# Kernel optimization log

Measured on AMD Instinct MI355X. Metric: run time of the kernel, lower is better.

## Reference

```python
import jax, jax.numpy as jnp
import numpy as np

B, H, W, C = 3072, 64, 64, 3  # kernel_size=64 forces H=W=64; reshape forces B % 3 == 0


def setup_inputs() -> dict:
    key = jax.random.key(0)
    k0, k1, k2, k3, k4 = jax.random.split(key, 5)
    inputs = jax.random.normal(k0, (B, H, W, C), dtype=jnp.float32)
    # Conv2D(filters=3, kernel_size=64) params, HWIO layout
    w1 = jax.random.normal(k1, (64, 64, 3, 3), dtype=jnp.float32) * 0.02
    b1 = jax.random.normal(k2, (3,), dtype=jnp.float32) * 0.02
    w2 = jax.random.normal(k3, (64, 64, 3, 3), dtype=jnp.float32) * 0.02
    b2 = jax.random.normal(k4, (3,), dtype=jnp.float32) * 0.02
    return {"inputs": inputs, "w1": w1, "b1": b1, "w2": w2, "b2": b2}


def _hilbert_axis1(x):
    # FFT-based Hilbert transform along axis=1 (analytic-signal filter), N even
    N = x.shape[1]
    h = np.zeros(N, dtype=np.float32)
    h[0] = h[N // 2] = 1.0
    h[1:N // 2] = 2.0
    hf = jnp.asarray(h)[None, :, None, None]
    Xf = jnp.fft.fft(x, axis=1)
    return jnp.imag(jnp.fft.ifft(Xf * hf, axis=1)).astype(x.dtype)


def reference(inputs, w1, b1, w2, b2):
    maps_x = inputs[..., :3]                                  # [B,64,64,3]
    b_, h_, w_, c_ = maps_x.shape
    # kernel covers the whole 64x64 image -> 1x1 conv output == full contraction
    v1 = jnp.einsum('bhwc,hwcf->bf', maps_x, w1) + b1          # [B,3]
    v2 = jnp.einsum('bhwc,hwcf->bf', maps_x, w2) + b2          # [B,3]
    V = jnp.stack([v1, v2], axis=-1)                           # [B,3,2]
    V = V / (1e-6 + jnp.sum(jnp.abs(V), axis=1, keepdims=True))
    mx_t = maps_x.reshape(b_, h_ * w_, c_).transpose(0, 2, 1)  # [B,3,HW]
    # Gram matrix and closed-form 2x2 inverse (math of tf.linalg.inv on [B,2,2])
    G = jnp.einsum('bci,bcj->bij', V, V)                       # [B,2,2]
    a = G[:, 0, 0]; bb = G[:, 0, 1]; c = G[:, 1, 0]; d = G[:, 1, 1]
    det = a * d - bb * c
    Ginv = jnp.stack([jnp.stack([d, -bb], -1),
                      jnp.stack([-c, a], -1)], 1) / det[:, None, None]  # [B,2,2]
    Vt_x = jnp.einsum('bck,bcn->bkn', V, mx_t)                 # [B,2,HW]
    rec_t = jnp.einsum('bck,bkn->bcn', V, Ginv @ Vt_x)         # [B,3,HW]
    # lstsq(V, rec_t) via normal equations (tf fast lstsq): z = Ginv V^T rec_t
    z = Ginv @ jnp.einsum('bck,bcn->bkn', V, rec_t)            # [B,2,HW]
    rec = z.transpose(0, 2, 1).reshape(-1, h_, w_, c_)         # [2B/3,64,64,3]
    rec_h = _hilbert_axis1(rec)
    return jnp.concatenate([rec, rec_h], axis=-1)              # [2B/3,64,64,6]
```

## Files before the change

### kernel.cpp

```cpp
#include <hip/hip_runtime.h>
#include <math.h>

#define B_TOT 3072
#define PIX   12288
#define BM    4

typedef float v2f __attribute__((ext_vector_type(2)));

__global__ __launch_bounds__(256) void compute_M_kernel(
    const float* __restrict__ x, const float* __restrict__ w1,
    const float* __restrict__ b1, const float* __restrict__ w2,
    const float* __restrict__ b2, float* __restrict__ Mout) {
  const int b0 = blockIdx.x * BM;
  const float4* __restrict__ w14 = (const float4*)w1;
  const float4* __restrict__ w24 = (const float4*)w2;
  const float4* __restrict__ xb4 = (const float4*)(x + (size_t)b0 * PIX);

  float acc[BM][6];
  #pragma unroll
  for (int b = 0; b < BM; ++b)
    #pragma unroll
    for (int f = 0; f < 6; ++f) acc[b][f] = 0.f;

  #pragma unroll 2
  for (int it = 0; it < PIX / 4 / 256; ++it) {
    const int i4 = threadIdx.x + it * 256;
    float4 a0 = w14[i4 * 3 + 0], a1 = w14[i4 * 3 + 1], a2 = w14[i4 * 3 + 2];
    float4 c0 = w24[i4 * 3 + 0], c1 = w24[i4 * 3 + 1], c2 = w24[i4 * 3 + 2];
    #pragma unroll
    for (int b = 0; b < BM; ++b) {
      float4 xv = xb4[(size_t)b * (PIX / 4) + i4];
      acc[b][0] += xv.x * a0.x + xv.y * a0.w + xv.z * a1.z + xv.w * a2.y;
      acc[b][1] += xv.x * a0.y + xv.y * a1.x + xv.z * a1.w + xv.w * a2.z;
      acc[b][2] += xv.x * a0.z + xv.y * a1.y + xv.z * a2.x + xv.w * a2.w;
      acc[b][3] += xv.x * c0.x + xv.y * c0.w + xv.z * c1.z + xv.w * c2.y;
      acc[b][4] += xv.x * c0.y + xv.y * c1.x + xv.z * c1.w + xv.w * c2.z;
      acc[b][5] += xv.x * c0.z + xv.y * c1.y + xv.z * c2.x + xv.w * c2.w;
    }
  }

  #pragma unroll
  for (int b = 0; b < BM; ++b)
    #pragma unroll
    for (int f = 0; f < 6; ++f)
      #pragma unroll
      for (int off = 32; off > 0; off >>= 1)
        acc[b][f] += __shfl_down(acc[b][f], off, 64);

  __shared__ float wred[4][BM][6];
  const int wave = threadIdx.x >> 6, lane = threadIdx.x & 63;
  if (lane == 0) {
    #pragma unroll
    for (int b = 0; b < BM; ++b)
      #pragma unroll
      for (int f = 0; f < 6; ++f) wred[wave][b][f] = acc[b][f];
  }
  __syncthreads();

  if (threadIdx.x < BM) {
    const int b = threadIdx.x;
    double v[3][2];
    for (int c = 0; c < 3; ++c) {
      v[c][0] = (double)wred[0][b][c] + (double)wred[1][b][c] +
                (double)wred[2][b][c] + (double)wred[3][b][c] + (double)b1[c];
      v[c][1] = (double)wred[0][b][3 + c] + (double)wred[1][b][3 + c] +
                (double)wred[2][b][3 + c] + (double)wred[3][b][3 + c] +
                (double)b2[c];
    }
    for (int k = 0; k < 2; ++k) {
      double l1 = 1e-6 + fabs(v[0][k]) + fabs(v[1][k]) + fabs(v[2][k]);
      for (int c = 0; c < 3; ++c) v[c][k] /= l1;
    }
    double G00 = 0, G01 = 0, G11 = 0;
    for (int c = 0; c < 3; ++c) {
      G00 += v[c][0] * v[c][0];
      G01 += v[c][0] * v[c][1];
      G11 += v[c][1] * v[c][1];
    }
    double det = G00 * G11 - G01 * G01;
    double i00 = G11 / det, i01 = -G01 / det, i11 = G00 / det;
    float* Mo = Mout + (size_t)(b0 + b) * 6;
    for (int c = 0; c < 3; ++c) {
      Mo[0 * 3 + c] = (float)(i00 * v[c][0] + i01 * v[c][1]);
      Mo[1 * 3 + c] = (float)(i01 * v[c][0] + i11 * v[c][1]);
    }
  }
}

__global__ __launch_bounds__(256) void z_hilbert_kernel(
    const float* __restrict__ x, const float* __restrict__ M,
    float* __restrict__ out) {
  const int b2 = blockIdx.x;
  __shared__ __align__(16) float rec[PIX];
  __shared__ float Ms[12];
  const size_t zbase = (size_t)b2 * PIX;
  const int b_lo = (int)(zbase >> 13);
  if (threadIdx.x < 12) {
    int bb = b_lo + (int)(threadIdx.x / 6);
    float mv = 0.f;
    if (bb < B_TOT) mv = M[(size_t)bb * 6 + (threadIdx.x % 6)];
    Ms[threadIdx.x] = mv;
  }
  __syncthreads();
  float* outb = out + (size_t)b2 * 24576;

  #pragma unroll
  for (int it = 0; it < 6; ++it) {
    int g = threadIdx.x + it * 256;
    int ml = g << 3;
    size_t m = zbase + (size_t)ml;
    int b = (int)(m >> 13);
    int n0 = (int)((m & 8191) >> 1);
    int wb = (b - b_lo) * 6;
    float m00 = Ms[wb + 0], m01 = Ms[wb + 1], m02 = Ms[wb + 2];
    float m10 = Ms[wb + 3], m11 = Ms[wb + 4], m12 = Ms[wb + 5];
    const float4* xp = (const float4*)(x + (size_t)b * PIX + (size_t)n0 * 3);
    float4 p0 = xp[0], p1 = xp[1], p2 = xp[2];
    float4 o0, o1;
    o0.x = m00 * p0.x + m01 * p0.y + m02 * p0.z;
    o0.y = m10 * p0.x + m11 * p0.y + m12 * p0.z;
    o0.z = m00 * p0.w + m01 * p1.x + m02 * p1.y;
    o0.w = m10 * p0.w + m11 * p1.x + m12 * p1.y;
    o1.x = m00 * p1.z + m01 * p1.w + m02 * p2.x;
    o1.y = m10 * p1.z + m11 * p1.w + m12 * p2.x;
    o1.z = m00 * p2.y + m01 * p2.z + m02 * p2.w;
    o1.w = m10 * p2.y + m11 * p2.z + m12 * p2.w;
    float4* rp = (float4*)&rec[ml];
    rp[0] = o0;
    rp[1] = o1;
  }
  __syncthreads();

  const int wave = threadIdx.x >> 6, lane = threadIdx.x & 63;
  if (lane < 48) {
    const int w = wave * 16 + lane / 3;
    const int c = lane % 3;
    const int col = w * 3 + c;
    float gc[16];
    #pragma unroll
    for (int jj = 0; jj < 16; ++jj) {
      float ang = 3.14159265358979323846f * (float)(2 * jj + 1) / 64.0f;
      gc[jj] = 0.03125f * cosf(ang) / sinf(ang);
    }
    float v[64];
    #pragma unroll
    for (int h = 0; h < 64; ++h) v[h] = rec[h * 192 + col];
    float* oc = outb + w * 6 + c * 2;
    #pragma unroll
    for (int h = 0; h < 64; ++h) {
      float acc = 0.f;
      #pragma unroll
      for (int jj = 0; jj < 16; ++jj) {
        int d = 2 * jj + 1;
        acc += gc[jj] * (v[(h - d) & 63] - v[(h + d) & 63]);
      }
      float r = v[h];
      float s1 = __shfl(r, lane + 1, 64);
      float s2 = __shfl(acc, lane - 1, 64);
      v2f st;
      st.x = (c == 0) ? r : ((c == 1) ? s1 : s2);
      st.y = (c == 0) ? s1 : ((c == 1) ? s2 : acc);
      __builtin_nontemporal_store(st, (v2f*)(oc + (size_t)h * 384));
    }
  }
}

extern "C" void kernel_launch(void* const* d_in, const int* in_sizes, int n_in,
                              void* d_out, int out_size, void* d_ws, size_t ws_size,
                              hipStream_t stream) {
  const float* x  = (const float*)d_in[0];
  const float* w1 = (const float*)d_in[1];
  const float* b1 = (const float*)d_in[2];
  const float* w2 = (const float*)d_in[3];
  const float* b2 = (const float*)d_in[4];
  float* out = (float*)d_out;
  float* M = (float*)d_ws;

  compute_M_kernel<<<B_TOT / BM, 256, 0, stream>>>(x, w1, b1, w2, b2, M);
  z_hilbert_kernel<<<2048, 256, 0, stream>>>(x, M, out);
}
```

Before: 343.9 us.

## Stage raw input tile in LDS and fuse projection into Hilbert column load

The z_hilbert kernel now copies the contiguous input slice for its block into shared memory with coalesced float4 loads held in registers, then each column thread applies the 2x3 projection on the fly while reading its 64 values. This removes the separate projection pass with its strided global gathers and one barrier. In exchange it uses more LDS (72KB instead of 48KB), which may lower occupancy, and adds per-element select logic to pick the projection of the correct batch.

Result: slower. 374.1 us (+8.8%).

```diff
diff --git a/kernel.cpp b/kernel.cpp
--- a/kernel.cpp
+++ b/kernel.cpp
@@ -91,60 +91,64 @@
     const float* __restrict__ x, const float* __restrict__ M,
     float* __restrict__ out) {
   const int b2 = blockIdx.x;
-  __shared__ __align__(16) float rec[PIX];
+  __shared__ __align__(16) float xl[18432];
   __shared__ float Ms[12];
   const size_t zbase = (size_t)b2 * PIX;
   const int b_lo = (int)(zbase >> 13);
-  if (threadIdx.x < 12) {
-    int bb = b_lo + (int)(threadIdx.x / 6);
-    float mv = 0.f;
-    if (bb < B_TOT) mv = M[(size_t)bb * 6 + (threadIdx.x % 6)];
-    Ms[threadIdx.x] = mv;
+
+  {
+    const float4* xs4 = (const float4*)(x + (size_t)(zbase >> 1) * 3);
+    float4* xl4 = (float4*)xl;
+    float4 t[18];
+    #pragma unroll
+    for (int j = 0; j < 18; ++j) t[j] = xs4[threadIdx.x + j * 256];
+    if (threadIdx.x < 12) {
+      int bb = b_lo + (int)(threadIdx.x / 6);
+      float mv = 0.f;
+      if (bb < B_TOT) mv = M[(size_t)bb * 6 + (threadIdx.x % 6)];
+      Ms[threadIdx.x] = mv;
+    }
+    #pragma unroll
+    for (int j = 0; j < 18; ++j) xl4[threadIdx.x + j * 256] = t[j];
   }
   __syncthreads();
+
   float* outb = out + (size_t)b2 * 24576;
-
-  #pragma unroll
-  for (int it = 0; it < 6; ++it) {
-    int g = threadIdx.x + it * 256;
-    int ml = g << 3;
-    size_t m = zbase + (size_t)ml;
-    int b = (int)(m >> 13);
-    int n0 = (int)((m & 8191) >> 1);
-    int wb = (b - b_lo) * 6;
-    float m00 = Ms[wb + 0], m01 = Ms[wb + 1], m02 = Ms[wb + 2];
-    float m10 = Ms[wb + 3], m11 = Ms[wb + 4], m12 = Ms[wb + 5];
-    const float4* xp = (const float4*)(x + (size_t)b * PIX + (size_t)n0 * 3);
-    float4 p0 = xp[0], p1 = xp[1], p2 = xp[2];
-    float4 o0, o1;
-    o0.x = m00 * p0.x + m01 * p0.y + m02 * p0.z;
-    o0.y = m10 * p0.x + m11 * p0.y + m12 * p0.z;
-    o0.z = m00 * p0.w + m01 * p1.x + m02 * p1.y;
-    o0.w = m10 * p0.w + m11 * p1.x + m12 * p1.y;
-    o1.x = m00 * p1.z + m01 * p1.w + m02 * p2.x;
-    o1.y = m10 * p1.z + m11 * p1.w + m12 * p2.x;
-    o1.z = m00 * p2.y + m01 * p2.z + m02 * p2.w;
-    o1.w = m10 * p2.y + m11 * p2.z + m12 * p2.w;
-    float4* rp = (float4*)&rec[ml];
-    rp[0] = o0;
-    rp[1] = o1;
-  }
-  __syncthreads();
 
   const int wave = threadIdx.x >> 6, lane = threadIdx.x & 63;
   if (lane < 48) {
     const int w = wave * 16 + lane / 3;
     const int c = lane % 3;
     const int col = w * 3 + c;
+    const int k = col & 1;
+    const int q = col >> 1;
+    const float mlo0 = Ms[k * 3 + 0], mlo1 = Ms[k * 3 + 1], mlo2 = Ms[k * 3 + 2];
+    const float mhi0 = Ms[6 + k * 3 + 0], mhi1 = Ms[6 + k * 3 + 1],
+                mhi2 = Ms[6 + k * 3 + 2];
+    const int r_th = 8192 - ((b2 & 1) << 12) - col;
+    const int h_sw = (r_th + 191) / 192;
+
     float gc[16];
     #pragma unroll
     for (int jj = 0; jj < 16; ++jj) {
       float ang = 3.14159265358979323846f * (float)(2 * jj + 1) / 64.0f;
       gc[jj] = 0.03125f * cosf(ang) / sinf(ang);
     }
+
     float v[64];
+    const float* xq = xl + 3 * q;
     #pragma unroll
-    for (int h = 0; h < 64; ++h) v[h] = rec[h * 192 + col];
+    for (int h = 0; h < 64; ++h) {
+      float x0 = xq[288 * h + 0];
+      float x1 = xq[288 * h + 1];
+      float x2 = xq[288 * h + 2];
+      bool hi = (h >= h_sw);
+      float m0 = hi ? mhi0 : mlo0;
+      float m1 = hi ? mhi1 : mlo1;
+      float m2 = hi ? mhi2 : mlo2;
+      v[h] = m0 * x0 + m1 * x1 + m2 * x2;
+    }
+
     float* oc = outb + w * 6 + c * 2;
     #pragma unroll
     for (int h = 0; h < 64; ++h) {
```
